# Optimization experiments

Hardware: AMD Instinct MI355X
Metric: run time of the kernel (lower is better)

Reference implementation:

```python
import jax, jax.numpy as jnp
import numpy as np

B, S, E = 2, 2048, 2048
H, D = 16, 128  # num_heads, head_dim; H*D == E
EPS = 1e-5


def setup_inputs() -> dict:
    key = jax.random.key(0)
    ks = jax.random.split(key, 9)
    s = 0.02
    return {
        "x": jax.random.normal(ks[0], (B, S, E), dtype=jnp.float32),
        "ln1_scale": jnp.ones((E,), dtype=jnp.float32),
        "Wq": jax.random.normal(ks[1], (E, H, D), dtype=jnp.float32) * s,
        "Wk": jax.random.normal(ks[2], (E, H, D), dtype=jnp.float32) * s,
        "Wv": jax.random.normal(ks[3], (E, H, D), dtype=jnp.float32) * s,
        "Wo": jax.random.normal(ks[4], (H, D, E), dtype=jnp.float32) * s,
        "ln2_scale": jnp.ones((E,), dtype=jnp.float32),
        "Wmlp": jax.random.normal(ks[5], (E, E), dtype=jnp.float32) * s,
        "bmlp": jnp.zeros((E,), dtype=jnp.float32),
    }


def _rmsnorm(x, scale, eps=EPS):
    var = jnp.mean(jnp.square(x), axis=-1, keepdims=True)
    return x * jax.lax.rsqrt(var + eps) * scale


def _causal_mha(x, Wq, Wk, Wv, Wo):
    # x: [B,S,E] -> q,k,v: [B,S,H,D]
    q = jnp.einsum("bse,ehd->bshd", x, Wq)
    k = jnp.einsum("bse,ehd->bshd", x, Wk)
    v = jnp.einsum("bse,ehd->bshd", x, Wv)
    scale = 1.0 / jnp.sqrt(jnp.float32(q.shape[-1]))
    scores = jnp.einsum("bqhd,bkhd->bhqk", q, k) * scale  # [B,H,S,S]
    causal = jnp.tril(jnp.ones((x.shape[1], x.shape[1]), dtype=bool))
    scores = jnp.where(causal[None, None], scores, jnp.finfo(scores.dtype).min)
    probs = jax.nn.softmax(scores, axis=-1)
    ctx = jnp.einsum("bhqk,bkhd->bqhd", probs, v)  # [B,S,H,D]
    return jnp.einsum("bqhd,hde->bqe", ctx, Wo)


def reference(x, ln1_scale, Wq, Wk, Wv, Wo, ln2_scale, Wmlp, bmlp):
    # TinyLlamaBlock, schedule[layer_id] == ANCHOR (full causal MHA), use_rope=False
    normed = _rmsnorm(x, ln1_scale)
    attn_out = _causal_mha(normed, Wq, Wk, Wv, Wo)
    x = x + attn_out
    x = x + (_rmsnorm(x, ln2_scale) @ Wmlp + bmlp)
    return x
```

## Files before the change

### kernel.cpp

```cpp
#include <hip/hip_runtime.h>


typedef unsigned short ushort_t;
typedef __attribute__((ext_vector_type(8))) short short8;
typedef __attribute__((ext_vector_type(4))) float floatx4;

__device__ __forceinline__ ushort_t f2bf(float f) {
  union { float f; unsigned u; } v; v.f = f;
  unsigned r = v.u + 0x7fffu + ((v.u >> 16) & 1u);
  return (ushort_t)(r >> 16);
}
__device__ __forceinline__ float bf2f(unsigned h) {
  union { unsigned u; float f; } v; v.u = h << 16; return v.f;
}
__device__ __forceinline__ void load16(const ushort_t* g, ushort_t* l) {
  __builtin_amdgcn_global_load_lds(
      (const __attribute__((address_space(1))) unsigned*)g,
      (__attribute__((address_space(3))) unsigned*)l, 16, 0, 0);
}

__global__ __launch_bounds__(256) void transpose_w_kernel(
    const float* __restrict__ src, ushort_t* __restrict__ dst) {
  __shared__ __align__(16) ushort_t tile[64][72];
  const int t = threadIdx.x;
  const int n0 = blockIdx.x * 64, k0 = blockIdx.y * 64;
#pragma unroll
  for (int i = 0; i < 4; ++i) {
    int c = t + 256 * i;
    int r = c >> 4, o = (c & 15) * 4;
    float4 raw = *(const float4*)&src[(size_t)(k0 + r) * 2048 + n0 + o];
    tile[o + 0][r] = f2bf(raw.x);
    tile[o + 1][r] = f2bf(raw.y);
    tile[o + 2][r] = f2bf(raw.z);
    tile[o + 3][r] = f2bf(raw.w);
  }
  __syncthreads();
#pragma unroll
  for (int i = 0; i < 2; ++i) {
    int c = t + 256 * i;
    int r = c >> 3, o = (c & 7) * 8;
    *(uint4*)&dst[(size_t)(n0 + r) * 2048 + k0 + o] = *(const uint4*)&tile[r][o];
  }
}

template <bool XBF>
__global__ __launch_bounds__(256) void rmsnorm_kernel(
    const void* __restrict__ xv, int in_ld, const float* __restrict__ g,
    ushort_t* __restrict__ out, int out_ld) {
  const int row = blockIdx.x, t = threadIdx.x;
  float v[8];
  if (XBF) {
    uint4 raw = *(const uint4*)((const ushort_t*)xv + (size_t)row * in_ld + t * 8);
    v[0] = bf2f(raw.x & 0xffffu); v[1] = bf2f(raw.x >> 16);
    v[2] = bf2f(raw.y & 0xffffu); v[3] = bf2f(raw.y >> 16);
    v[4] = bf2f(raw.z & 0xffffu); v[5] = bf2f(raw.z >> 16);
    v[6] = bf2f(raw.w & 0xffffu); v[7] = bf2f(raw.w >> 16);
  } else {
    const float* xr = (const float*)xv + (size_t)row * in_ld + t * 8;
    float4 a = *(const float4*)xr;
    float4 b = *(const float4*)(xr + 4);
    v[0] = a.x; v[1] = a.y; v[2] = a.z; v[3] = a.w;
    v[4] = b.x; v[5] = b.y; v[6] = b.z; v[7] = b.w;
  }
  float ss = 0.f;
#pragma unroll
  for (int i = 0; i < 8; ++i) ss += v[i] * v[i];
#pragma unroll
  for (int m = 32; m >= 1; m >>= 1) ss += __shfl_xor(ss, m, 64);
  __shared__ float red[4];
  if ((t & 63) == 0) red[t >> 6] = ss;
  __syncthreads();
  float rs = rsqrtf((red[0] + red[1] + red[2] + red[3]) * (1.0f / 2048.0f) + 1e-5f);
  const float* gp = g + t * 8;
  float4 ga = *(const float4*)gp;
  float4 gb = *(const float4*)(gp + 4);
  float gv[8] = {ga.x, ga.y, ga.z, ga.w, gb.x, gb.y, gb.z, gb.w};
  union { ushort_t u16[8]; uint4 u; } p;
#pragma unroll
  for (int i = 0; i < 8; ++i) p.u16[i] = f2bf(v[i] * rs * gv[i]);
  *(uint4*)&out[(size_t)row * out_ld + t * 8] = p.u;
}

template <int MODE>
__global__ __launch_bounds__(256, 2) void gemm_bt(
    const ushort_t* A, int lda, const ushort_t* Bt, int ldb,
    void* Cv, int ldc, const void* resid, int ldr,
    const float* bias, int M, int N, int K) {
  __shared__ __align__(16) ushort_t As[128][32];
  __shared__ __align__(16) ushort_t Bs[128][32];
  const int t = threadIdx.x;
  const int wid = t >> 6, lane = t & 63;
  const int l15 = lane & 15, quad = lane >> 4;
  const int m0 = blockIdx.y * 128, n0 = blockIdx.x * 128;
  const int wm = (wid >> 1) * 64, wn = (wid & 1) * 64;

  const int srow = wid * 32 + (lane >> 2);
  const int scol = (lane & 3) * 8;
  const ushort_t* ag0 = &A[(size_t)(m0 + srow) * lda + scol];
  const ushort_t* ag1 = &A[(size_t)(m0 + srow + 16) * lda + scol];
  const ushort_t* bg0 = &Bt[(size_t)(n0 + srow) * ldb + scol];
  const ushort_t* bg1 = &Bt[(size_t)(n0 + srow + 16) * ldb + scol];
  ushort_t* al0 = &As[wid * 32][0];
  ushort_t* al1 = &As[wid * 32 + 16][0];
  ushort_t* bl0 = &Bs[wid * 32][0];
  ushort_t* bl1 = &Bs[wid * 32 + 16][0];

  floatx4 acc[4][4];
#pragma unroll
  for (int i = 0; i < 4; ++i)
#pragma unroll
    for (int j = 0; j < 4; ++j) acc[i][j] = (floatx4){0.f, 0.f, 0.f, 0.f};

  for (int k0 = 0; k0 < K; k0 += 32) {
    __syncthreads();
    load16(ag0 + k0, al0);
    load16(ag1 + k0, al1);
    load16(bg0 + k0, bl0);
    load16(bg1 + k0, bl1);
    __syncthreads();

    short8 af[4], bf[4];
#pragma unroll
    for (int i = 0; i < 4; ++i)
      af[i] = *(const short8*)&As[wm + i * 16 + l15][quad * 8];
#pragma unroll
    for (int j = 0; j < 4; ++j)
      bf[j] = *(const short8*)&Bs[wn + j * 16 + l15][quad * 8];
#pragma unroll
    for (int i = 0; i < 4; ++i)
#pragma unroll
      for (int j = 0; j < 4; ++j)
        acc[i][j] = __builtin_amdgcn_mfma_f32_16x16x32_bf16(af[i], bf[j],
                                                            acc[i][j], 0, 0, 0);
  }

#pragma unroll
  for (int i = 0; i < 4; ++i)
#pragma unroll
    for (int j = 0; j < 4; ++j)
#pragma unroll
      for (int r = 0; r < 4; ++r) {
        int row = m0 + wm + i * 16 + quad * 4 + r;
        int col = n0 + wn + j * 16 + l15;
        float v = acc[i][j][r];
        if (MODE == 0) {
          ((ushort_t*)Cv)[(size_t)row * ldc + col] = f2bf(v);
        } else if (MODE == 1) {
          float rv = ((const float*)resid)[(size_t)row * ldr + col];
          ((ushort_t*)Cv)[(size_t)row * ldc + col] = f2bf(rv + v);
        } else {
          float rv = bf2f(((const ushort_t*)resid)[(size_t)row * ldr + col]);
          ((float*)Cv)[(size_t)row * ldc + col] = rv + v + bias[col];
        }
      }
}

__global__ __launch_bounds__(256) void transpose_v_kernel(
    const ushort_t* __restrict__ qkv, ushort_t* __restrict__ vT) {
  __shared__ __align__(16) ushort_t tile[64][72];
  const int t = threadIdx.x;
  const int s0 = blockIdx.x * 64, d0 = blockIdx.y * 64;
  const int bh = blockIdx.z, b = bh >> 4, h = bh & 15;
#pragma unroll
  for (int i = 0; i < 2; ++i) {
    int c = t + 256 * i, r = c >> 3, o = (c & 7) * 8;
    uint4 raw = *(const uint4*)&qkv[(size_t)(b * 2048 + s0 + r) * 6144 + 4096 +
                                    h * 128 + d0 + o];
    tile[o + 0][r] = (ushort_t)(raw.x & 0xffffu);
    tile[o + 1][r] = (ushort_t)(raw.x >> 16);
    tile[o + 2][r] = (ushort_t)(raw.y & 0xffffu);
    tile[o + 3][r] = (ushort_t)(raw.y >> 16);
    tile[o + 4][r] = (ushort_t)(raw.z & 0xffffu);
    tile[o + 5][r] = (ushort_t)(raw.z >> 16);
    tile[o + 6][r] = (ushort_t)(raw.w & 0xffffu);
    tile[o + 7][r] = (ushort_t)(raw.w >> 16);
  }
  __syncthreads();
#pragma unroll
  for (int i = 0; i < 2; ++i) {
    int c = t + 256 * i, r = c >> 3, o = (c & 7) * 8;
    *(uint4*)&vT[((size_t)bh * 128 + d0 + r) * 2048 + s0 + o] =
        *(const uint4*)&tile[r][o];
  }
}

__global__ __launch_bounds__(256, 3) void attn_kernel(
    const ushort_t* qkv, const ushort_t* vT, ushort_t* ctx, int ldctx) {
  const int S = 2048, LD = 6144, D = 128;
  __shared__ __align__(16) ushort_t Ks[64][136];
  __shared__ __align__(16) ushort_t Vt[128][72];
  __shared__ __align__(16) ushort_t Ps[4][16][72];
  const int t = threadIdx.x;
  const int wid = t >> 6, lane = t & 63;
  const int l15 = lane & 15, quad = lane >> 4;
  const int bh = blockIdx.y, b = bh >> 4, h = bh & 15;

  const int krow = t >> 4, kcol = (t & 15) * 8;
  const int vrow = t >> 3, vcol = (t & 7) * 8;
  const ushort_t* kgp = &qkv[(size_t)(b * S + krow) * LD + 2048 + h * D + kcol];
  const ushort_t* vgp = &vT[((size_t)bh * D + vrow) * S + vcol];

  uint4 k0r, k1r, k2r, k3r, v0r, v1r, v2r, v3r;
#define PREFETCH(KB)                                          \
  do {                                                        \
    const ushort_t* kp_ = kgp + (size_t)(KB)*LD;              \
    k0r = *(const uint4*)(kp_);                               \
    k1r = *(const uint4*)(kp_ + (size_t)16 * LD);             \
    k2r = *(const uint4*)(kp_ + (size_t)32 * LD);             \
    k3r = *(const uint4*)(kp_ + (size_t)48 * LD);             \
    const ushort_t* vp_ = vgp + (KB);                         \
    v0r = *(const uint4*)(vp_);                               \
    v1r = *(const uint4*)(vp_ + (size_t)32 * S);              \
    v2r = *(const uint4*)(vp_ + (size_t)64 * S);              \
    v3r = *(const uint4*)(vp_ + (size_t)96 * S);              \
  } while (0)

  const float sc = 0.08838834764831845f;

  for (int ph = 0; ph < 2; ++ph) {
    const int qtile = ph == 0 ? (31 - (int)blockIdx.x) : (int)blockIdx.x;
    const int qb = qtile * 64;

    short8 qf[4];
    {
      const ushort_t* qp =
          &qkv[(size_t)(b * S + qb + wid * 16 + l15) * LD + h * D];
#pragma unroll
      for (int kk = 0; kk < 4; ++kk)
        qf[kk] = *(const short8*)&qp[kk * 32 + quad * 8];
    }

    floatx4 accO[8];
#pragma unroll
    for (int i = 0; i < 8; ++i) accO[i] = (floatx4){0.f, 0.f, 0.f, 0.f};
    float m_i = -1e30f;
    float l_i = 0.f;
    const int qg = qb + wid * 16 + l15;

    const int nkt = qtile + 1;
    PREFETCH(0);
    for (int kt = 0; kt < nkt; ++kt) {
      const int kb = kt * 64;
      __syncthreads();
      *(uint4*)&Ks[krow + 0][kcol]  = k0r;
      *(uint4*)&Ks[krow + 16][kcol] = k1r;
      *(uint4*)&Ks[krow + 32][kcol] = k2r;
      *(uint4*)&Ks[krow + 48][kcol] = k3r;
      *(uint4*)&Vt[vrow + 0][vcol]  = v0r;
      *(uint4*)&Vt[vrow + 32][vcol] = v1r;
      *(uint4*)&Vt[vrow + 64][vcol] = v2r;
      *(uint4*)&Vt[vrow + 96][vcol] = v3r;
      __syncthreads();
      if (kt + 1 < nkt) {
        PREFETCH(kb + 64);
      } else if (ph == 0) {
        PREFETCH(0);
      }

      floatx4 st[4];
#pragma unroll
      for (int jn = 0; jn < 4; ++jn) {
        st[jn] = (floatx4){0.f, 0.f, 0.f, 0.f};
#pragma unroll
        for (int kk = 0; kk < 4; ++kk) {
          short8 kf = *(const short8*)&Ks[jn * 16 + l15][kk * 32 + quad * 8];
          st[jn] = __builtin_amdgcn_mfma_f32_16x16x32_bf16(kf, qf[kk], st[jn], 0, 0, 0);
        }
      }

      float p[4][4];
#pragma unroll
      for (int jn = 0; jn < 4; ++jn)
#pragma unroll
        for (int r = 0; r < 4; ++r) {
          int kg = kb + jn * 16 + quad * 4 + r;
          float s = st[jn][r] * sc;
          p[jn][r] = (kg <= qg) ? s : -1e30f;
        }

      float mq0 = fmaxf(fmaxf(p[0][0], p[0][1]), fmaxf(p[0][2], p[0][3]));
      float mq1 = fmaxf(fmaxf(p[1][0], p[1][1]), fmaxf(p[1][2], p[1][3]));
      float mq2 = fmaxf(fmaxf(p[2][0], p[2][1]), fmaxf(p[2][2], p[2][3]));
      float mq3 = fmaxf(fmaxf(p[3][0], p[3][1]), fmaxf(p[3][2], p[3][3]));
      float v = fmaxf(fmaxf(mq0, mq1), fmaxf(mq2, mq3));
      v = fmaxf(v, __shfl_xor(v, 16, 64));
      v = fmaxf(v, __shfl_xor(v, 32, 64));
      float mnew = fmaxf(m_i, v);
      float alpha = __expf(m_i - mnew);
      m_i = mnew;

      float arow[4];
#pragma unroll
      for (int r = 0; r < 4; ++r) arow[r] = __shfl(alpha, quad * 4 + r, 16);

#pragma unroll
      for (int jn = 0; jn < 4; ++jn)
#pragma unroll
        for (int r = 0; r < 4; ++r) p[jn][r] = __expf(p[jn][r] - m_i);

#pragma unroll
      for (int jn = 0; jn < 4; ++jn) {
        union { ushort_t h[4]; uint2 v2; } pk;
#pragma unroll
        for (int r = 0; r < 4; ++r) pk.h[r] = f2bf(p[jn][r]);
        *(uint2*)&Ps[wid][l15][jn * 16 + quad * 4] = pk.v2;
      }

      float sq = ((p[0][0] + p[0][1]) + (p[0][2] + p[0][3])) +
                 ((p[1][0] + p[1][1]) + (p[1][2] + p[1][3])) +
                 ((p[2][0] + p[2][1]) + (p[2][2] + p[2][3])) +
                 ((p[3][0] + p[3][1]) + (p[3][2] + p[3][3]));
      sq += __shfl_xor(sq, 16, 64);
      sq += __shfl_xor(sq, 32, 64);
      l_i = l_i * alpha + sq;

#pragma unroll
      for (int jd = 0; jd < 8; ++jd)
#pragma unroll
        for (int r = 0; r < 4; ++r) accO[jd][r] *= arow[r];

      __asm__ __volatile__("s_waitcnt lgkmcnt(0)" ::: "memory");

      short8 pf[2];
#pragma unroll
      for (int kk = 0; kk < 2; ++kk)
        pf[kk] = *(const short8*)&Ps[wid][l15][kk * 32 + quad * 8];
#pragma unroll
      for (int jd = 0; jd < 8; ++jd)
#pragma unroll
        for (int kk = 0; kk < 2; ++kk) {
          short8 vf = *(const short8*)&Vt[jd * 16 + l15][kk * 32 + quad * 8];
          accO[jd] = __builtin_amdgcn_mfma_f32_16x16x32_bf16(pf[kk], vf, accO[jd], 0, 0, 0);
        }
    }

    float lrow[4];
#pragma unroll
    for (int r = 0; r < 4; ++r) lrow[r] = 1.0f / __shfl(l_i, quad * 4 + r, 16);
#pragma unroll
    for (int jd = 0; jd < 8; ++jd)
#pragma unroll
      for (int r = 0; r < 4; ++r) {
        int row = b * S + qb + wid * 16 + quad * 4 + r;
        int col = h * D + jd * 16 + l15;
        ctx[(size_t)row * ldctx + col] = f2bf(accO[jd][r] * lrow[r]);
      }
  }
#undef PREFETCH
}

extern "C" void kernel_launch(void* const* d_in, const int* in_sizes, int n_in,
                              void* d_out, int out_size, void* d_ws,
                              size_t ws_size, hipStream_t stream) {
  const float* x    = (const float*)d_in[0];
  const float* ln1  = (const float*)d_in[1];
  const float* Wq   = (const float*)d_in[2];
  const float* Wk   = (const float*)d_in[3];
  const float* Wv   = (const float*)d_in[4];
  const float* Wo   = (const float*)d_in[5];
  const float* ln2  = (const float*)d_in[6];
  const float* Wmlp = (const float*)d_in[7];
  const float* bmlp = (const float*)d_in[8];
  float* out = (float*)d_out;

  char* ws = (char*)d_ws;
  ushort_t* qkv = (ushort_t*)(ws + 0);
  ushort_t* R2  = (ushort_t*)(ws + 50331648);
  ushort_t* WqT   = R2;
  ushort_t* WkT   = R2 + 4194304;
  ushort_t* WvT   = R2;
  ushort_t* vT    = R2;
  ushort_t* WoT   = R2;
  ushort_t* WmlpT = R2;
  ushort_t* n1  = (ushort_t*)d_out;
  ushort_t* ctx = qkv + 4096;
  ushort_t* x1  = qkv + 2048;
  ushort_t* n2  = qkv;

  dim3 blk(256);
  dim3 tgrid(32, 32);
  dim3 ggrid(16, 32);
  dim3 ggridQK(32, 32);

  rmsnorm_kernel<false><<<dim3(4096), blk, 0, stream>>>(x, 2048, ln1, n1, 2048);

  transpose_w_kernel<<<tgrid, blk, 0, stream>>>(Wq, WqT);
  transpose_w_kernel<<<tgrid, blk, 0, stream>>>(Wk, WkT);
  gemm_bt<0><<<ggridQK, blk, 0, stream>>>(n1, 2048, WqT, 2048, qkv + 0, 6144,
                                          nullptr, 0, nullptr, 4096, 4096, 2048);
  transpose_w_kernel<<<tgrid, blk, 0, stream>>>(Wv, WvT);
  gemm_bt<0><<<ggrid, blk, 0, stream>>>(n1, 2048, WvT, 2048, qkv + 4096, 6144,
                                        nullptr, 0, nullptr, 4096, 2048, 2048);

  transpose_v_kernel<<<dim3(32, 2, 32), blk, 0, stream>>>(qkv, vT);

  attn_kernel<<<dim3(16, 32), blk, 0, stream>>>(qkv, vT, ctx, 6144);

  transpose_w_kernel<<<tgrid, blk, 0, stream>>>(Wo, WoT);
  gemm_bt<1><<<ggrid, blk, 0, stream>>>(ctx, 6144, WoT, 2048, x1, 6144,
                                        x, 2048, nullptr, 4096, 2048, 2048);

  rmsnorm_kernel<true><<<dim3(4096), blk, 0, stream>>>(x1, 6144, ln2, n2, 6144);

  transpose_w_kernel<<<tgrid, blk, 0, stream>>>(Wmlp, WmlpT);
  gemm_bt<2><<<ggrid, blk, 0, stream>>>(n2, 6144, WmlpT, 2048, out, 2048,
                                        x1, 6144, bmlp, 4096, 2048, 2048);
}
```

Baseline: 504.0 us.

## Fuse QKV GEMM launches and double-buffer attention K/V tiles with lazy rescaling

The Q/K and V projection GEMMs become one launch: blocks with column offset past 4096 read a second transposed weight pointer, and WvT moves into spare space in the output buffer. The attention kernel double-buffers K/V in LDS and prefetches across the two phases, removing one barrier per tile. It also applies the causal mask only on the last tile, folds log2(e) into the scale to use exp2, and skips the accumulator rescale when the new max exceeds the old by at most 8. P is packed to bf16 with a hardware convert instruction. The larger LDS footprint lowers occupancy from 3 to 2 blocks, and the deferred rescale allows unnormalised values up to 2^8, which is a small numerical risk.

```diff
diff --git a/kernel.cpp b/kernel.cpp
--- a/kernel.cpp
+++ b/kernel.cpp
@@ -83,8 +83,8 @@
 
 template <int MODE>
 __global__ __launch_bounds__(256, 2) void gemm_bt(
-    const ushort_t* A, int lda, const ushort_t* Bt, int ldb,
-    void* Cv, int ldc, const void* resid, int ldr,
+    const ushort_t* A, int lda, const ushort_t* Bt, const ushort_t* Bt2,
+    int ldb, void* Cv, int ldc, const void* resid, int ldr,
     const float* bias, int M, int N, int K) {
   __shared__ __align__(16) ushort_t As[128][32];
   __shared__ __align__(16) ushort_t Bs[128][32];
@@ -94,12 +94,16 @@
   const int m0 = blockIdx.y * 128, n0 = blockIdx.x * 128;
   const int wm = (wid >> 1) * 64, wn = (wid & 1) * 64;
 
+  const ushort_t* btb = Bt;
+  int nr = n0;
+  if (Bt2 != nullptr && n0 >= 4096) { btb = Bt2; nr = n0 - 4096; }
+
   const int srow = wid * 32 + (lane >> 2);
   const int scol = (lane & 3) * 8;
   const ushort_t* ag0 = &A[(size_t)(m0 + srow) * lda + scol];
   const ushort_t* ag1 = &A[(size_t)(m0 + srow + 16) * lda + scol];
-  const ushort_t* bg0 = &Bt[(size_t)(n0 + srow) * ldb + scol];
-  const ushort_t* bg1 = &Bt[(size_t)(n0 + srow + 16) * ldb + scol];
+  const ushort_t* bg0 = &btb[(size_t)(nr + srow) * ldb + scol];
+  const ushort_t* bg1 = &btb[(size_t)(nr + srow + 16) * ldb + scol];
   ushort_t* al0 = &As[wid * 32][0];
   ushort_t* al1 = &As[wid * 32 + 16][0];
   ushort_t* bl0 = &Bs[wid * 32][0];
@@ -184,15 +188,16 @@
   }
 }
 
-__global__ __launch_bounds__(256, 3) void attn_kernel(
+__global__ __launch_bounds__(256, 2) void attn_kernel(
     const ushort_t* qkv, const ushort_t* vT, ushort_t* ctx, int ldctx) {
   const int S = 2048, LD = 6144, D = 128;
-  __shared__ __align__(16) ushort_t Ks[64][136];
-  __shared__ __align__(16) ushort_t Vt[128][72];
+  __shared__ __align__(16) ushort_t Ks[2][64][136];
+  __shared__ __align__(16) ushort_t Vt[2][128][72];
   __shared__ __align__(16) ushort_t Ps[4][16][72];
   const int t = threadIdx.x;
   const int wid = t >> 6, lane = t & 63;
   const int l15 = lane & 15, quad = lane >> 4;
+  const int bx = (int)blockIdx.x;
   const int bh = blockIdx.y, b = bh >> 4, h = bh & 15;
 
   const int krow = t >> 4, kcol = (t & 15) * 8;
@@ -214,11 +219,29 @@
     v2r = *(const uint4*)(vp_ + (size_t)64 * S);              \
     v3r = *(const uint4*)(vp_ + (size_t)96 * S);              \
   } while (0)
-
-  const float sc = 0.08838834764831845f;
-
+#define STAGE(BUF)                                            \
+  do {                                                        \
+    *(uint4*)&Ks[BUF][krow + 0][kcol]  = k0r;                 \
+    *(uint4*)&Ks[BUF][krow + 16][kcol] = k1r;                 \
+    *(uint4*)&Ks[BUF][krow + 32][kcol] = k2r;                 \
+    *(uint4*)&Ks[BUF][krow + 48][kcol] = k3r;                 \
+    *(uint4*)&Vt[BUF][vrow + 0][vcol]  = v0r;                 \
+    *(uint4*)&Vt[BUF][vrow + 32][vcol] = v1r;                 \
+    *(uint4*)&Vt[BUF][vrow + 64][vcol] = v2r;                 \
+    *(uint4*)&Vt[BUF][vrow + 96][vcol] = v3r;                 \
+  } while (0)
+
+  const float sc2 = 0.08838834764831845f * 1.4426950408889634f;
+  const int nkt0 = 32 - bx;
+  const int NT = 33;
+
+  PREFETCH(0);
+  STAGE(0);
+  PREFETCH(64);
+
+  int g = 0;
   for (int ph = 0; ph < 2; ++ph) {
-    const int qtile = ph == 0 ? (31 - (int)blockIdx.x) : (int)blockIdx.x;
+    const int qtile = ph == 0 ? (31 - bx) : bx;
     const int qb = qtile * 64;
 
     short8 qf[4];
@@ -238,23 +261,17 @@
     const int qg = qb + wid * 16 + l15;
 
     const int nkt = qtile + 1;
-    PREFETCH(0);
-    for (int kt = 0; kt < nkt; ++kt) {
+    for (int kt = 0; kt < nkt; ++kt, ++g) {
       const int kb = kt * 64;
+      const int buf = g & 1;
       __syncthreads();
-      *(uint4*)&Ks[krow + 0][kcol]  = k0r;
-      *(uint4*)&Ks[krow + 16][kcol] = k1r;
-      *(uint4*)&Ks[krow + 32][kcol] = k2r;
-      *(uint4*)&Ks[krow + 48][kcol] = k3r;
-      *(uint4*)&Vt[vrow + 0][vcol]  = v0r;
-      *(uint4*)&Vt[vrow + 32][vcol] = v1r;
-      *(uint4*)&Vt[vrow + 64][vcol] = v2r;
-      *(uint4*)&Vt[vrow + 96][vcol] = v3r;
-      __syncthreads();
-      if (kt + 1 < nkt) {
-        PREFETCH(kb + 64);
-      } else if (ph == 0) {
-        PREFETCH(0);
+      if (g + 1 < NT) {
+        STAGE(buf ^ 1);
+        if (g + 2 < NT) {
+          const int g2 = g + 2;
+          const int kb2 = (g2 < nkt0) ? g2 * 64 : (g2 - nkt0) * 64;
+          PREFETCH(kb2);
+        }
       }
 
       floatx4 st[4];
@@ -263,20 +280,27 @@
         st[jn] = (floatx4){0.f, 0.f, 0.f, 0.f};
 #pragma unroll
         for (int kk = 0; kk < 4; ++kk) {
-          short8 kf = *(const short8*)&Ks[jn * 16 + l15][kk * 32 + quad * 8];
+          short8 kf = *(const short8*)&Ks[buf][jn * 16 + l15][kk * 32 + quad * 8];
           st[jn] = __builtin_amdgcn_mfma_f32_16x16x32_bf16(kf, qf[kk], st[jn], 0, 0, 0);
         }
       }
 
       float p[4][4];
-#pragma unroll
-      for (int jn = 0; jn < 4; ++jn)
-#pragma unroll
-        for (int r = 0; r < 4; ++r) {
-          int kg = kb + jn * 16 + quad * 4 + r;
-          float s = st[jn][r] * sc;
-          p[jn][r] = (kg <= qg) ? s : -1e30f;
-        }
+      if (kt == nkt - 1) {
+#pragma unroll
+        for (int jn = 0; jn < 4; ++jn)
+#pragma unroll
+          for (int r = 0; r < 4; ++r) {
+            int kg = kb + jn * 16 + quad * 4 + r;
+            float s = st[jn][r] * sc2;
+            p[jn][r] = (kg <= qg) ? s : -1e30f;
+          }
+      } else {
+#pragma unroll
+        for (int jn = 0; jn < 4; ++jn)
+#pragma unroll
+          for (int r = 0; r < 4; ++r) p[jn][r] = st[jn][r] * sc2;
+      }
 
       float mq0 = fmaxf(fmaxf(p[0][0], p[0][1]), fmaxf(p[0][2], p[0][3]));
       float mq1 = fmaxf(fmaxf(p[1][0], p[1][1]), fmaxf(p[1][2], p[1][3]));
@@ -285,25 +309,35 @@
       float v = fmaxf(fmaxf(mq0, mq1), fmaxf(mq2, mq3));
       v = fmaxf(v, __shfl_xor(v, 16, 64));
       v = fmaxf(v, __shfl_xor(v, 32, 64));
-      float mnew = fmaxf(m_i, v);
-      float alpha = __expf(m_i - mnew);
-      m_i = mnew;
-
-      float arow[4];
-#pragma unroll
-      for (int r = 0; r < 4; ++r) arow[r] = __shfl(alpha, quad * 4 + r, 16);
+
+      if (!__all(v - m_i <= 8.0f)) {
+        float mnew = fmaxf(m_i, v);
+        float alpha = exp2f(m_i - mnew);
+        m_i = mnew;
+        float arow[4];
+#pragma unroll
+        for (int r = 0; r < 4; ++r) arow[r] = __shfl(alpha, quad * 4 + r, 16);
+#pragma unroll
+        for (int jd = 0; jd < 8; ++jd)
+#pragma unroll
+          for (int r = 0; r < 4; ++r) accO[jd][r] *= arow[r];
+        l_i *= alpha;
+      }
 
 #pragma unroll
       for (int jn = 0; jn < 4; ++jn)
 #pragma unroll
-        for (int r = 0; r < 4; ++r) p[jn][r] = __expf(p[jn][r] - m_i);
+        for (int r = 0; r < 4; ++r) p[jn][r] = exp2f(p[jn][r] - m_i);
 
 #pragma unroll
       for (int jn = 0; jn < 4; ++jn) {
-        union { ushort_t h[4]; uint2 v2; } pk;
-#pragma unroll
-        for (int r = 0; r < 4; ++r) pk.h[r] = f2bf(p[jn][r]);
-        *(uint2*)&Ps[wid][l15][jn * 16 + quad * 4] = pk.v2;
+        unsigned w0, w1;
+        asm("v_cvt_pk_bf16_f32 %0, %1, %2" : "=v"(w0)
+            : "v"(p[jn][0]), "v"(p[jn][1]));
+        asm("v_cvt_pk_bf16_f32 %0, %1, %2" : "=v"(w1)
+            : "v"(p[jn][2]), "v"(p[jn][3]));
+        uint2 pk2; pk2.x = w0; pk2.y = w1;
+        *(uint2*)&Ps[wid][l15][jn * 16 + quad * 4] = pk2;
       }
 
       float sq = ((p[0][0] + p[0][1]) + (p[0][2] + p[0][3])) +
@@ -312,12 +346,7 @@
                  ((p[3][0] + p[3][1]) + (p[3][2] + p[3][3]));
       sq += __shfl_xor(sq, 16, 64);
       sq += __shfl_xor(sq, 32, 64);
-      l_i = l_i * alpha + sq;
-
-#pragma unroll
-      for (int jd = 0; jd < 8; ++jd)
-#pragma unroll
-        for (int r = 0; r < 4; ++r) accO[jd][r] *= arow[r];
+      l_i += sq;
 
       __asm__ __volatile__("s_waitcnt lgkmcnt(0)" ::: "memory");
 
@@ -329,7 +358,7 @@
       for (int jd = 0; jd < 8; ++jd)
 #pragma unroll
         for (int kk = 0; kk < 2; ++kk) {
-          short8 vf = *(const short8*)&Vt[jd * 16 + l15][kk * 32 + quad * 8];
+          short8 vf = *(const short8*)&Vt[buf][jd * 16 + l15][kk * 32 + quad * 8];
           accO[jd] = __builtin_amdgcn_mfma_f32_16x16x32_bf16(pf[kk], vf, accO[jd], 0, 0, 0);
         }
     }
@@ -347,6 +376,7 @@
       }
   }
 #undef PREFETCH
+#undef STAGE
 }
 
 extern "C" void kernel_launch(void* const* d_in, const int* in_sizes, int n_in,
@@ -368,11 +398,11 @@
   ushort_t* R2  = (ushort_t*)(ws + 50331648);
   ushort_t* WqT   = R2;
   ushort_t* WkT   = R2 + 4194304;
-  ushort_t* WvT   = R2;
   ushort_t* vT    = R2;
   ushort_t* WoT   = R2;
   ushort_t* WmlpT = R2;
   ushort_t* n1  = (ushort_t*)d_out;
+  ushort_t* WvT = (ushort_t*)d_out + 8388608;
   ushort_t* ctx = qkv + 4096;
   ushort_t* x1  = qkv + 2048;
   ushort_t* n2  = qkv;
@@ -380,29 +410,27 @@
   dim3 blk(256);
   dim3 tgrid(32, 32);
   dim3 ggrid(16, 32);
-  dim3 ggridQK(32, 32);
+  dim3 ggridQKV(48, 32);
 
   rmsnorm_kernel<false><<<dim3(4096), blk, 0, stream>>>(x, 2048, ln1, n1, 2048);
 
   transpose_w_kernel<<<tgrid, blk, 0, stream>>>(Wq, WqT);
   transpose_w_kernel<<<tgrid, blk, 0, stream>>>(Wk, WkT);
-  gemm_bt<0><<<ggridQK, blk, 0, stream>>>(n1, 2048, WqT, 2048, qkv + 0, 6144,
-                                          nullptr, 0, nullptr, 4096, 4096, 2048);
   transpose_w_kernel<<<tgrid, blk, 0, stream>>>(Wv, WvT);
-  gemm_bt<0><<<ggrid, blk, 0, stream>>>(n1, 2048, WvT, 2048, qkv + 4096, 6144,
-                                        nullptr, 0, nullptr, 4096, 2048, 2048);
+  gemm_bt<0><<<ggridQKV, blk, 0, stream>>>(n1, 2048, WqT, WvT, 2048, qkv, 6144,
+                                           nullptr, 0, nullptr, 4096, 6144, 2048);
 
   transpose_v_kernel<<<dim3(32, 2, 32), blk, 0, stream>>>(qkv, vT);
 
   attn_kernel<<<dim3(16, 32), blk, 0, stream>>>(qkv, vT, ctx, 6144);
 
   transpose_w_kernel<<<tgrid, blk, 0, stream>>>(Wo, WoT);
-  gemm_bt<1><<<ggrid, blk, 0, stream>>>(ctx, 6144, WoT, 2048, x1, 6144,
+  gemm_bt<1><<<ggrid, blk, 0, stream>>>(ctx, 6144, WoT, nullptr, 2048, x1, 6144,
                                         x, 2048, nullptr, 4096, 2048, 2048);
 
   rmsnorm_kernel<true><<<dim3(4096), blk, 0, stream>>>(x1, 6144, ln2, n2, 6144);
 
   transpose_w_kernel<<<tgrid, blk, 0, stream>>>(Wmlp, WmlpT);
-  gemm_bt<2><<<ggrid, blk, 0, stream>>>(n2, 6144, WmlpT, 2048, out, 2048,
+  gemm_bt<2><<<ggrid, blk, 0, stream>>>(n2, 6144, WmlpT, nullptr, 2048, out, 2048,
                                         x1, 6144, bmlp, 4096, 2048, 2048);
 }
```

After: 493.1 us. -2.2%, faster.
